# Optimization experiments

Measured on AMD Instinct MI355X. Metric: run time of the kernel, lower is better.

## Reference

```python
import jax, jax.numpy as jnp
import numpy as np

N_NODES = 50000
N_EDGES = 800000
N_GRAPHS = 64
IN_C = 256      # num_commodities
HID = 256       # hidden_units
HID2 = HID // 2
N_DCS = 64


def setup_inputs() -> dict:
    key = jax.random.key(0)
    ks = jax.random.split(key, 8)
    x = jax.random.normal(ks[0], (N_NODES, IN_C), dtype=jnp.float32)
    edge_index = jax.random.randint(ks[1], (2, N_EDGES), 0, N_NODES, dtype=jnp.int32)
    # sorted graph-membership ids; even partition guarantees no empty graph
    batch = ((jnp.arange(N_NODES) * N_GRAPHS) // N_NODES).astype(jnp.int32)
    s1 = 1.0 / np.sqrt(IN_C)
    s2 = 1.0 / np.sqrt(HID)
    s3 = 1.0 / np.sqrt(HID2)
    W1 = jax.random.normal(ks[2], (IN_C, HID), dtype=jnp.float32) * s1
    b1 = jnp.zeros((HID,), dtype=jnp.float32)
    W2 = jax.random.normal(ks[3], (HID, HID2), dtype=jnp.float32) * s2
    b2 = jnp.zeros((HID2,), dtype=jnp.float32)
    Wm = jax.random.normal(ks[4], (HID2, N_DCS), dtype=jnp.float32) * s3
    bm = jax.random.normal(ks[5], (N_DCS,), dtype=jnp.float32) * s3
    return {"x": x, "edge_index": edge_index, "batch": batch,
            "W1": W1, "b1": b1, "W2": W2, "b2": b2, "Wm": Wm, "bm": bm}


def gcn_conv(x, W, b, src, dst, n_nodes):
    """PyG GCNConv: D^{-1/2}(A+I)D^{-1/2} X W + b (self-loops added)."""
    h = x @ W                                    # [N, out]
    ones = jnp.ones(src.shape[0], dtype=h.dtype)
    deg = jax.ops.segment_sum(ones, dst, num_segments=n_nodes) + 1.0  # +1 self-loop
    dis = jax.lax.rsqrt(deg)                     # deg >= 1, safe
    norm = dis[src] * dis[dst]                   # [E]
    agg = jax.ops.segment_sum(h[src] * norm[:, None], dst, num_segments=n_nodes)
    agg = agg + h * (dis * dis)[:, None]         # self-loop contribution
    return agg + b


def reference(x, edge_index, batch, W1, b1, W2, b2, Wm, bm):
    src, dst = edge_index[0], edge_index[1]
    n = x.shape[0]
    bx = jax.nn.relu(gcn_conv(x, W1, b1, src, dst, n))
    cx = jax.nn.relu(gcn_conv(bx, W2, b2, src, dst, n))
    px = jax.ops.segment_max(cx, batch, num_segments=N_GRAPHS)  # global max pool
    return px @ Wm + bm                           # [N_GRAPHS, N_DCS]
```

## Files before the change

### kernel.cpp

```cpp
#include <hip/hip_runtime.h>
#include <cstdint>


typedef _Float16 half2v __attribute__((ext_vector_type(2)));
typedef _Float16 half4v __attribute__((ext_vector_type(4)));
typedef _Float16 half8v __attribute__((ext_vector_type(8)));
typedef float f32x4 __attribute__((ext_vector_type(4)));

#define CAP 64

__device__ __forceinline__ void gl_lds16(const void* g, void* l) {
  __builtin_amdgcn_global_load_lds(
      (const __attribute__((address_space(1))) unsigned int*)g,
      (__attribute__((address_space(3))) unsigned int*)l, 16, 0, 0);
}

__global__ void cvtW_k(const float* __restrict__ W1, _Float16* __restrict__ Wt1,
                       const float* __restrict__ W2, _Float16* __restrict__ Wt2) {
  int i = blockIdx.x * 256 + threadIdx.x;
  if (i < 256 * 256) {
    int k = i >> 8, c = i & 255;
    Wt1[c * 256 + k] = (_Float16)W1[i];
  } else {
    int j = i - 256 * 256;
    if (j < 256 * 128) {
      int k = j >> 7, c = j & 127;
      Wt2[c * 256 + k] = (_Float16)W2[j];
    }
  }
}

__global__ void fill_slots_k(const int* __restrict__ src, const int* __restrict__ dst,
                             int* __restrict__ cnt, unsigned short* __restrict__ slots,
                             int E) {
  int i = blockIdx.x * blockDim.x + threadIdx.x;
  int e0 = i * 4;
  if (e0 + 4 <= E) {
    int4 d = *(const int4*)(dst + e0);
    int4 s = *(const int4*)(src + e0);
    int p0 = atomicAdd(&cnt[d.x << 4], 1);
    if (p0 < CAP) slots[(d.x << 6) + p0] = (unsigned short)s.x;
    int p1 = atomicAdd(&cnt[d.y << 4], 1);
    if (p1 < CAP) slots[(d.y << 6) + p1] = (unsigned short)s.y;
    int p2 = atomicAdd(&cnt[d.z << 4], 1);
    if (p2 < CAP) slots[(d.z << 6) + p2] = (unsigned short)s.z;
    int p3 = atomicAdd(&cnt[d.w << 4], 1);
    if (p3 < CAP) slots[(d.w << 6) + p3] = (unsigned short)s.w;
  } else {
    for (int e = e0; e < E; ++e) {
      int d = dst[e];
      int p = atomicAdd(&cnt[d << 4], 1);
      if (p < CAP) slots[(d << 6) + p] = (unsigned short)src[e];
    }
  }
}

__global__ __launch_bounds__(256) void gemm1_k(const float* __restrict__ A,
                                               const _Float16* __restrict__ Bt,
                                               const int* __restrict__ cnt,
                                               _Float16* __restrict__ C, int M) {
  constexpr int K = 256, N = 256, BM = 64, BK = 32;
  __shared__ _Float16 As[BM * BK];
  __shared__ _Float16 Bs[N * BK];
  const int tid = threadIdx.x, lane = tid & 63, wave = tid >> 6;
  const int row0 = blockIdx.x * BM;
  const int kbase = (lane >> 4) * 8;
  const int r16 = lane & 15;

  int arow = row0 + wave * 16 + r16;
  if (arow > M - 1) arow = M - 1;
  const float* aSrc = A + (size_t)arow * K + kbase;
  _Float16* aDst = As + wave * 512 + lane * 8;

  const _Float16* bSrc[4];
  _Float16* bDst[4];
#pragma unroll
  for (int hh = 0; hh < 4; ++hh) {
    int fl = hh * 4 + wave;
    bSrc[hh] = Bt + (size_t)(fl * 16 + r16) * K + kbase;
    bDst[hh] = Bs + fl * 512;
  }

  f32x4 acc[4][4] = {};
  for (int k0 = 0; k0 < K; k0 += BK) {
#pragma unroll
    for (int hh = 0; hh < 4; ++hh) gl_lds16(bSrc[hh] + k0, bDst[hh]);
    float4 a0 = *(const float4*)(aSrc + k0);
    float4 a1 = *(const float4*)(aSrc + k0 + 4);
    half8v ah = {(_Float16)a0.x, (_Float16)a0.y, (_Float16)a0.z, (_Float16)a0.w,
                 (_Float16)a1.x, (_Float16)a1.y, (_Float16)a1.z, (_Float16)a1.w};
    *(half8v*)aDst = ah;
    __syncthreads();

    half8v af[4], bf[4];
#pragma unroll
    for (int m = 0; m < 4; ++m)
      af[m] = *(const half8v*)(As + m * 512 + lane * 8);
#pragma unroll
    for (int nj = 0; nj < 4; ++nj)
      bf[nj] = *(const half8v*)(Bs + (wave * 4 + nj) * 512 + lane * 8);
#pragma unroll
    for (int m = 0; m < 4; ++m)
#pragma unroll
      for (int nj = 0; nj < 4; ++nj)
        acc[m][nj] = __builtin_amdgcn_mfma_f32_16x16x32_f16(af[m], bf[nj], acc[m][nj], 0, 0, 0);
    __syncthreads();
  }

#pragma unroll
  for (int m = 0; m < 4; ++m) {
    const int rbase = row0 + m * 16 + (lane >> 4) * 4;
    float dr[4];
#pragma unroll
    for (int r = 0; r < 4; ++r)
      dr[r] = (rbase + r < M) ? rsqrtf((float)cnt[(rbase + r) << 4] + 1.0f) : 0.f;
#pragma unroll
    for (int nj = 0; nj < 4; ++nj) {
      int col = wave * 64 + nj * 16 + r16;
#pragma unroll
      for (int r = 0; r < 4; ++r) {
        int row = rbase + r;
        if (row < M) C[(size_t)row * N + col] = (_Float16)(acc[m][nj][r] * dr[r]);
      }
    }
  }
}

#define GBM 128
#define GBN 128
#define GBK 32

__global__ __launch_bounds__(256) void gemm_f16(const _Float16* __restrict__ A,
                                                const _Float16* __restrict__ Bt,
                                                const int* __restrict__ cnt,
                                                _Float16* __restrict__ C,
                                                int M, int N, int K) {
  __shared__ _Float16 As[GBM * GBK];
  __shared__ _Float16 Bs[GBN * GBK];
  const int tid = threadIdx.x;
  const int lane = tid & 63;
  const int wave = tid >> 6;
  const int wm = wave >> 1, wn = wave & 1;
  const int row0 = blockIdx.x * GBM;
  const int col0 = blockIdx.y * GBN;

  f32x4 acc[4][4] = {};

  const int kbase = (lane >> 4) * 8;
  const _Float16* aSrc[2];
  _Float16* aDst[2];
  const _Float16* bSrc[2];
  _Float16* bDst[2];
#pragma unroll
  for (int h = 0; h < 2; ++h) {
    int fl = h * 4 + wave;
    int row = h * 64 + wave * 16 + (lane & 15);
    int gr = row0 + row;
    if (gr > M - 1) gr = M - 1;
    aSrc[h] = A + (size_t)gr * K + kbase;
    aDst[h] = As + fl * 512;
    int gc = col0 + row;
    bSrc[h] = Bt + (size_t)gc * K + kbase;
    bDst[h] = Bs + fl * 512;
  }

  for (int k0 = 0; k0 < K; k0 += GBK) {
    gl_lds16(aSrc[0] + k0, aDst[0]);
    gl_lds16(aSrc[1] + k0, aDst[1]);
    gl_lds16(bSrc[0] + k0, bDst[0]);
    gl_lds16(bSrc[1] + k0, bDst[1]);
    __syncthreads();

    half8v af[4], bf[4];
#pragma unroll
    for (int m = 0; m < 4; ++m)
      af[m] = *(const half8v*)(As + (wm * 4 + m) * 512 + lane * 8);
#pragma unroll
    for (int nj = 0; nj < 4; ++nj)
      bf[nj] = *(const half8v*)(Bs + (wn * 4 + nj) * 512 + lane * 8);
#pragma unroll
    for (int m = 0; m < 4; ++m)
#pragma unroll
      for (int nj = 0; nj < 4; ++nj)
        acc[m][nj] = __builtin_amdgcn_mfma_f32_16x16x32_f16(af[m], bf[nj], acc[m][nj], 0, 0, 0);
    __syncthreads();
  }

#pragma unroll
  for (int m = 0; m < 4; ++m) {
    const int rbase = row0 + wm * 64 + m * 16 + (lane >> 4) * 4;
    float dr[4];
#pragma unroll
    for (int r = 0; r < 4; ++r)
      dr[r] = (rbase + r < M) ? rsqrtf((float)cnt[(rbase + r) << 4] + 1.0f) : 0.f;
#pragma unroll
    for (int nj = 0; nj < 4; ++nj) {
      int col = col0 + wn * 64 + nj * 16 + (lane & 15);
#pragma unroll
      for (int r = 0; r < 4; ++r) {
        int row = rbase + r;
        if (row < M) C[(size_t)row * N + col] = (_Float16)(acc[m][nj][r] * dr[r]);
      }
    }
  }
}

template <int C, bool POOL>
__global__ __launch_bounds__(256) void agg_k(const _Float16* __restrict__ h,
                                             const int* __restrict__ cnt,
                                             const unsigned short* __restrict__ slots,
                                             const float* __restrict__ bias,
                                             const int* __restrict__ batch,
                                             void* __restrict__ outv, int n) {
  constexpr int LPR = C / 8;
  constexpr int EPW = 64 / LPR;
  constexpr int U = 8;
  constexpr int EBLK = EPW * U;
  const int tid = threadIdx.x;
  const int lane = tid & 63;
  const int wave = tid >> 6;
  const int slot = lane / LPR;
  const int ch0 = (lane % LPR) * 8;

  const int wid = blockIdx.x * 4 + wave;
  const bool valid = wid < n;
  const int node = valid ? wid : n - 1;

  const int rawc = cnt[node << 4];
  const int end = rawc < CAP ? rawc : CAP;
  const unsigned short* nsl = slots + (node << 6);

  float acc[8] = {};
  int jb = 0;
  for (; jb + EBLK <= end; jb += EBLK) {
    half2v ah0[4] = {}, ah1[4] = {};
#pragma unroll
    for (int u = 0; u < U; ++u) {
      int s = nsl[jb + u * EPW + slot];
      half8v hv = *(const half8v*)(h + (size_t)s * C + ch0);
      const half2v* hp = (const half2v*)&hv;
      if (u < 4) {
#pragma unroll
        for (int p = 0; p < 4; ++p) ah0[p] += hp[p];
      } else {
#pragma unroll
        for (int p = 0; p < 4; ++p) ah1[p] += hp[p];
      }
    }
#pragma unroll
    for (int p = 0; p < 4; ++p) {
      acc[2 * p + 0] += (float)ah0[p][0] + (float)ah1[p][0];
      acc[2 * p + 1] += (float)ah0[p][1] + (float)ah1[p][1];
    }
  }
  if (jb < end) {
    half2v ah0[4] = {}, ah1[4] = {};
#pragma unroll
    for (int u = 0; u < U; ++u) {
      int e = jb + u * EPW + slot;
      bool ok = e < end;
      int s = nsl[ok ? e : end - 1];
      half8v hv = *(const half8v*)(h + (size_t)s * C + ch0);
      if (!ok) hv = half8v{};
      const half2v* hp = (const half2v*)&hv;
      if (u < 4) {
#pragma unroll
        for (int p = 0; p < 4; ++p) ah0[p] += hp[p];
      } else {
#pragma unroll
        for (int p = 0; p < 4; ++p) ah1[p] += hp[p];
      }
    }
#pragma unroll
    for (int p = 0; p < 4; ++p) {
      acc[2 * p + 0] += (float)ah0[p][0] + (float)ah1[p][0];
      acc[2 * p + 1] += (float)ah0[p][1] + (float)ah1[p][1];
    }
  }

  if constexpr (EPW == 4) {
#pragma unroll
    for (int v = 0; v < 8; ++v) {
      acc[v] += __shfl_xor(acc[v], 16);
      acc[v] += __shfl_xor(acc[v], 32);
    }
  } else {
#pragma unroll
    for (int v = 0; v < 8; ++v) acc[v] += __shfl_xor(acc[v], 32);
  }

  const float di = rsqrtf((float)rawc + 1.0f);
  half8v sv = *(const half8v*)(h + (size_t)node * C + ch0);
  float4 blo = *(const float4*)(bias + ch0);
  float4 bhi = *(const float4*)(bias + ch0 + 4);
  const float bb[8] = {blo.x, blo.y, blo.z, blo.w, bhi.x, bhi.y, bhi.z, bhi.w};
  float res[8];
#pragma unroll
  for (int v = 0; v < 8; ++v)
    res[v] = fmaxf((acc[v] + (float)sv[v]) * di + bb[v], 0.f);

  if constexpr (!POOL) {
    if (valid && lane < LPR) {
      half8v r;
#pragma unroll
      for (int v = 0; v < 8; ++v) r[v] = (_Float16)res[v];
      *(half8v*)((_Float16*)outv + (size_t)node * C + ch0) = r;
    }
  } else {
    __shared__ float pres[4][C];
    __shared__ int pg[4];
    __shared__ int uni;
    const int g = valid ? batch[node] : -1 - wave;
    if (lane < LPR) {
      *(f32x4*)&pres[wave][ch0] = f32x4{res[0], res[1], res[2], res[3]};
      *(f32x4*)&pres[wave][ch0 + 4] = f32x4{res[4], res[5], res[6], res[7]};
    }
    if (lane == 0) pg[wave] = g;
    __syncthreads();
    if (tid == 0) uni = (pg[0] == pg[1] && pg[1] == pg[2] && pg[2] == pg[3] && pg[0] >= 0);
    __syncthreads();
    float* px = (float*)outv;
    if (uni) {
      if (tid < C) {
        float m = fmaxf(fmaxf(pres[0][tid], pres[1][tid]),
                        fmaxf(pres[2][tid], pres[3][tid]));
        atomicMax((int*)&px[(size_t)pg[0] * C + tid], __float_as_int(m));
      }
    } else {
#pragma unroll
      for (int wv = 0; wv < 4; ++wv) {
        int gg = pg[wv];
        if (gg >= 0 && tid < C)
          atomicMax((int*)&px[(size_t)gg * C + tid], __float_as_int(pres[wv][tid]));
      }
    }
  }
}

__global__ void final_mm_k(const float* __restrict__ px, const float* __restrict__ Wm,
                           const float* __restrict__ bm, float* __restrict__ out) {
  int g = blockIdx.x;
  int c = threadIdx.x;
  float acc = bm[c];
#pragma unroll 8
  for (int k = 0; k < 128; ++k)
    acc = fmaf(px[g * 128 + k], Wm[k * 64 + c], acc);
  out[g * 64 + c] = acc;
}

extern "C" void kernel_launch(void* const* d_in, const int* in_sizes, int n_in,
                              void* d_out, int out_size, void* d_ws, size_t ws_size,
                              hipStream_t stream) {
  const float* x     = (const float*)d_in[0];
  const int*   ei    = (const int*)d_in[1];
  const int*   batch = (const int*)d_in[2];
  const float* W1    = (const float*)d_in[3];
  const float* b1    = (const float*)d_in[4];
  const float* W2    = (const float*)d_in[5];
  const float* b2    = (const float*)d_in[6];
  const float* Wm    = (const float*)d_in[7];
  const float* bm    = (const float*)d_in[8];
  float* out = (float*)d_out;

  const int E = in_sizes[1] / 2;
  const int n = in_sizes[2];
  const int HID = 256, HID2 = 128, NG = 64;
  const int* src = ei;
  const int* dst = ei + E;

  char* w = (char*)d_ws;
  size_t off = 0;
  auto alloc = [&](size_t bytes) -> void* {
    void* p = w + off;
    off = (off + bytes + 255) & ~(size_t)255;
    return p;
  };
  int*            cnt    = (int*)alloc((size_t)n * 16 * 4);
  float*          px     = (float*)alloc((size_t)NG * HID2 * 4);
  size_t          zlen   = off;
  unsigned short* slots  = (unsigned short*)alloc((size_t)n * CAP * 2);
  _Float16*       Wt1    = (_Float16*)alloc((size_t)HID * 256 * 2);
  _Float16*       Wt2    = (_Float16*)alloc((size_t)HID2 * HID * 2);
  _Float16*       bufA   = (_Float16*)alloc((size_t)n * HID * 2);
  _Float16*       bufB   = (_Float16*)alloc((size_t)n * HID * 2);
  _Float16* h1 = bufA;
  _Float16* bx = bufB;
  _Float16* h2 = bufA;

  hipMemsetAsync(cnt, 0, zlen, stream);

  cvtW_k<<<(256 * 256 + 256 * 128 + 255) / 256, 256, 0, stream>>>(W1, Wt1, W2, Wt2);
  fill_slots_k<<<(E / 4 + 255) / 256, 256, 0, stream>>>(src, dst, cnt, slots, E);

  gemm1_k<<<(n + 63) / 64, 256, 0, stream>>>(x, Wt1, cnt, h1, n);
  agg_k<256, false><<<(n + 3) / 4, 256, 0, stream>>>(h1, cnt, slots, b1, nullptr, bx, n);

  dim3 g2((n + GBM - 1) / GBM, HID2 / GBN);
  gemm_f16<<<g2, 256, 0, stream>>>(bx, Wt2, cnt, h2, n, HID2, HID);
  agg_k<128, true><<<(n + 3) / 4, 256, 0, stream>>>(h2, cnt, slots, b2, batch, px, n);

  final_mm_k<<<NG, 64, 0, stream>>>(px, Wm, bm, out);
}
```

Baseline: 311.7 us.

## Shrink GEMM row tiles to 32 and simplify slot fill to one edge per thread

```diff
diff --git a/kernel.cpp b/kernel.cpp
--- a/kernel.cpp
+++ b/kernel.cpp
@@ -33,33 +33,19 @@
 __global__ void fill_slots_k(const int* __restrict__ src, const int* __restrict__ dst,
                              int* __restrict__ cnt, unsigned short* __restrict__ slots,
                              int E) {
-  int i = blockIdx.x * blockDim.x + threadIdx.x;
-  int e0 = i * 4;
-  if (e0 + 4 <= E) {
-    int4 d = *(const int4*)(dst + e0);
-    int4 s = *(const int4*)(src + e0);
-    int p0 = atomicAdd(&cnt[d.x << 4], 1);
-    if (p0 < CAP) slots[(d.x << 6) + p0] = (unsigned short)s.x;
-    int p1 = atomicAdd(&cnt[d.y << 4], 1);
-    if (p1 < CAP) slots[(d.y << 6) + p1] = (unsigned short)s.y;
-    int p2 = atomicAdd(&cnt[d.z << 4], 1);
-    if (p2 < CAP) slots[(d.z << 6) + p2] = (unsigned short)s.z;
-    int p3 = atomicAdd(&cnt[d.w << 4], 1);
-    if (p3 < CAP) slots[(d.w << 6) + p3] = (unsigned short)s.w;
-  } else {
-    for (int e = e0; e < E; ++e) {
-      int d = dst[e];
-      int p = atomicAdd(&cnt[d << 4], 1);
-      if (p < CAP) slots[(d << 6) + p] = (unsigned short)src[e];
-    }
-  }
+  int e = blockIdx.x * blockDim.x + threadIdx.x;
+  if (e >= E) return;
+  int d = dst[e];
+  int s = src[e];
+  int p = atomicAdd(&cnt[d << 4], 1);
+  if (p < CAP) slots[(d << 6) + p] = (unsigned short)s;
 }
 
 __global__ __launch_bounds__(256) void gemm1_k(const float* __restrict__ A,
                                                const _Float16* __restrict__ Bt,
                                                const int* __restrict__ cnt,
                                                _Float16* __restrict__ C, int M) {
-  constexpr int K = 256, N = 256, BM = 64, BK = 32;
+  constexpr int K = 256, N = 256, BM = 32, BK = 32;
   __shared__ _Float16 As[BM * BK];
   __shared__ _Float16 Bs[N * BK];
   const int tid = threadIdx.x, lane = tid & 63, wave = tid >> 6;
@@ -67,11 +53,6 @@
   const int kbase = (lane >> 4) * 8;
   const int r16 = lane & 15;
 
-  int arow = row0 + wave * 16 + r16;
-  if (arow > M - 1) arow = M - 1;
-  const float* aSrc = A + (size_t)arow * K + kbase;
-  _Float16* aDst = As + wave * 512 + lane * 8;
-
   const _Float16* bSrc[4];
   _Float16* bDst[4];
 #pragma unroll
@@ -81,26 +62,38 @@
     bDst[hh] = Bs + fl * 512;
   }
 
-  f32x4 acc[4][4] = {};
+  const bool doA = tid < 128;
+  const float* aSrc = nullptr;
+  _Float16* aDst = nullptr;
+  if (doA) {
+    int arow = row0 + (tid >> 2);
+    if (arow > M - 1) arow = M - 1;
+    aSrc = A + (size_t)arow * K + (tid & 3) * 8;
+    aDst = As + (tid >> 6) * 512 + (((tid & 3) << 4) + ((tid >> 2) & 15)) * 8;
+  }
+
+  f32x4 acc[2][4] = {};
   for (int k0 = 0; k0 < K; k0 += BK) {
 #pragma unroll
     for (int hh = 0; hh < 4; ++hh) gl_lds16(bSrc[hh] + k0, bDst[hh]);
-    float4 a0 = *(const float4*)(aSrc + k0);
-    float4 a1 = *(const float4*)(aSrc + k0 + 4);
-    half8v ah = {(_Float16)a0.x, (_Float16)a0.y, (_Float16)a0.z, (_Float16)a0.w,
-                 (_Float16)a1.x, (_Float16)a1.y, (_Float16)a1.z, (_Float16)a1.w};
-    *(half8v*)aDst = ah;
-    __syncthreads();
-
-    half8v af[4], bf[4];
-#pragma unroll
-    for (int m = 0; m < 4; ++m)
+    if (doA) {
+      float4 a0 = *(const float4*)(aSrc + k0);
+      float4 a1 = *(const float4*)(aSrc + k0 + 4);
+      half8v ah = {(_Float16)a0.x, (_Float16)a0.y, (_Float16)a0.z, (_Float16)a0.w,
+                   (_Float16)a1.x, (_Float16)a1.y, (_Float16)a1.z, (_Float16)a1.w};
+      *(half8v*)aDst = ah;
+    }
+    __syncthreads();
+
+    half8v af[2], bf[4];
+#pragma unroll
+    for (int m = 0; m < 2; ++m)
       af[m] = *(const half8v*)(As + m * 512 + lane * 8);
 #pragma unroll
     for (int nj = 0; nj < 4; ++nj)
       bf[nj] = *(const half8v*)(Bs + (wave * 4 + nj) * 512 + lane * 8);
 #pragma unroll
-    for (int m = 0; m < 4; ++m)
+    for (int m = 0; m < 2; ++m)
 #pragma unroll
       for (int nj = 0; nj < 4; ++nj)
         acc[m][nj] = __builtin_amdgcn_mfma_f32_16x16x32_f16(af[m], bf[nj], acc[m][nj], 0, 0, 0);
@@ -108,7 +101,7 @@
   }
 
 #pragma unroll
-  for (int m = 0; m < 4; ++m) {
+  for (int m = 0; m < 2; ++m) {
     const int rbase = row0 + m * 16 + (lane >> 4) * 4;
     float dr[4];
 #pragma unroll
@@ -126,80 +119,72 @@
   }
 }
 
-#define GBM 128
-#define GBN 128
-#define GBK 32
-
-__global__ __launch_bounds__(256) void gemm_f16(const _Float16* __restrict__ A,
-                                                const _Float16* __restrict__ Bt,
-                                                const int* __restrict__ cnt,
-                                                _Float16* __restrict__ C,
-                                                int M, int N, int K) {
-  __shared__ _Float16 As[GBM * GBK];
-  __shared__ _Float16 Bs[GBN * GBK];
-  const int tid = threadIdx.x;
-  const int lane = tid & 63;
-  const int wave = tid >> 6;
-  const int wm = wave >> 1, wn = wave & 1;
-  const int row0 = blockIdx.x * GBM;
-  const int col0 = blockIdx.y * GBN;
-
-  f32x4 acc[4][4] = {};
-
+__global__ __launch_bounds__(256) void gemm2_k(const _Float16* __restrict__ A,
+                                               const _Float16* __restrict__ Bt,
+                                               const int* __restrict__ cnt,
+                                               _Float16* __restrict__ C, int M) {
+  constexpr int K = 256, N = 128, BM = 32, BK = 32;
+  __shared__ _Float16 As[BM * BK];
+  __shared__ _Float16 Bs[N * BK];
+  const int tid = threadIdx.x, lane = tid & 63, wave = tid >> 6;
+  const int row0 = blockIdx.x * BM;
   const int kbase = (lane >> 4) * 8;
-  const _Float16* aSrc[2];
-  _Float16* aDst[2];
+  const int r16 = lane & 15;
+
   const _Float16* bSrc[2];
   _Float16* bDst[2];
 #pragma unroll
-  for (int h = 0; h < 2; ++h) {
-    int fl = h * 4 + wave;
-    int row = h * 64 + wave * 16 + (lane & 15);
-    int gr = row0 + row;
-    if (gr > M - 1) gr = M - 1;
-    aSrc[h] = A + (size_t)gr * K + kbase;
-    aDst[h] = As + fl * 512;
-    int gc = col0 + row;
-    bSrc[h] = Bt + (size_t)gc * K + kbase;
-    bDst[h] = Bs + fl * 512;
-  }
-
-  for (int k0 = 0; k0 < K; k0 += GBK) {
-    gl_lds16(aSrc[0] + k0, aDst[0]);
-    gl_lds16(aSrc[1] + k0, aDst[1]);
+  for (int hh = 0; hh < 2; ++hh) {
+    int fl = hh * 4 + wave;
+    bSrc[hh] = Bt + (size_t)(fl * 16 + r16) * K + kbase;
+    bDst[hh] = Bs + fl * 512;
+  }
+
+  const _Float16* aSrc = nullptr;
+  _Float16* aDst = nullptr;
+  if (wave < 2) {
+    int arow = row0 + wave * 16 + r16;
+    if (arow > M - 1) arow = M - 1;
+    aSrc = A + (size_t)arow * K + kbase;
+    aDst = As + wave * 512;
+  }
+
+  f32x4 acc[2][2] = {};
+  for (int k0 = 0; k0 < K; k0 += BK) {
     gl_lds16(bSrc[0] + k0, bDst[0]);
     gl_lds16(bSrc[1] + k0, bDst[1]);
-    __syncthreads();
-
-    half8v af[4], bf[4];
-#pragma unroll
-    for (int m = 0; m < 4; ++m)
-      af[m] = *(const half8v*)(As + (wm * 4 + m) * 512 + lane * 8);
-#pragma unroll
-    for (int nj = 0; nj < 4; ++nj)
-      bf[nj] = *(const half8v*)(Bs + (wn * 4 + nj) * 512 + lane * 8);
-#pragma unroll
-    for (int m = 0; m < 4; ++m)
-#pragma unroll
-      for (int nj = 0; nj < 4; ++nj)
-        acc[m][nj] = __builtin_amdgcn_mfma_f32_16x16x32_f16(af[m], bf[nj], acc[m][nj], 0, 0, 0);
-    __syncthreads();
-  }
-
-#pragma unroll
-  for (int m = 0; m < 4; ++m) {
-    const int rbase = row0 + wm * 64 + m * 16 + (lane >> 4) * 4;
+    if (wave < 2) gl_lds16(aSrc + k0, aDst);
+    __syncthreads();
+
+    half8v af[2], bf[2];
+#pragma unroll
+    for (int m = 0; m < 2; ++m)
+      af[m] = *(const half8v*)(As + m * 512 + lane * 8);
+#pragma unroll
+    for (int j = 0; j < 2; ++j)
+      bf[j] = *(const half8v*)(Bs + (wave * 2 + j) * 512 + lane * 8);
+#pragma unroll
+    for (int m = 0; m < 2; ++m)
+#pragma unroll
+      for (int j = 0; j < 2; ++j)
+        acc[m][j] = __builtin_amdgcn_mfma_f32_16x16x32_f16(af[m], bf[j], acc[m][j], 0, 0, 0);
+    __syncthreads();
+  }
+
+#pragma unroll
+  for (int m = 0; m < 2; ++m) {
+    const int rbase = row0 + m * 16 + (lane >> 4) * 4;
     float dr[4];
 #pragma unroll
     for (int r = 0; r < 4; ++r)
       dr[r] = (rbase + r < M) ? rsqrtf((float)cnt[(rbase + r) << 4] + 1.0f) : 0.f;
 #pragma unroll
-    for (int nj = 0; nj < 4; ++nj) {
-      int col = col0 + wn * 64 + nj * 16 + (lane & 15);
+    for (int j = 0; j < 2; ++j) {
+      int col = wave * 32 + j * 16 + r16;
 #pragma unroll
       for (int r = 0; r < 4; ++r) {
         int row = rbase + r;
-        if (row < M) C[(size_t)row * N + col] = (_Float16)(acc[m][nj][r] * dr[r]);
+        if (row < M) C[(size_t)row * N + col] = (_Float16)(acc[m][j][r] * dr[r]);
       }
     }
   }
@@ -390,13 +375,12 @@
   hipMemsetAsync(cnt, 0, zlen, stream);
 
   cvtW_k<<<(256 * 256 + 256 * 128 + 255) / 256, 256, 0, stream>>>(W1, Wt1, W2, Wt2);
-  fill_slots_k<<<(E / 4 + 255) / 256, 256, 0, stream>>>(src, dst, cnt, slots, E);
-
-  gemm1_k<<<(n + 63) / 64, 256, 0, stream>>>(x, Wt1, cnt, h1, n);
+  fill_slots_k<<<(E + 255) / 256, 256, 0, stream>>>(src, dst, cnt, slots, E);
+
+  gemm1_k<<<(n + 31) / 32, 256, 0, stream>>>(x, Wt1, cnt, h1, n);
   agg_k<256, false><<<(n + 3) / 4, 256, 0, stream>>>(h1, cnt, slots, b1, nullptr, bx, n);
 
-  dim3 g2((n + GBM - 1) / GBM, HID2 / GBN);
-  gemm_f16<<<g2, 256, 0, stream>>>(bx, Wt2, cnt, h2, n, HID2, HID);
+  gemm2_k<<<(n + 31) / 32, 256, 0, stream>>>(bx, Wt2, cnt, h2, n);
   agg_k<128, true><<<(n + 3) / 4, 256, 0, stream>>>(h2, cnt, slots, b2, batch, px, n);
 
   final_mm_k<<<NG, 64, 0, stream>>>(px, Wm, bm, out);
```

After: 309.6 us. Within noise of the previous version (-0.7%).
